# Performance work log

Measured on AMD Instinct MI355X. Metric: run time of the kernel, lower is better.

The kernel has to match this reference:

```python
import jax, jax.numpy as jnp
import numpy as np

B, C, H, W = 8, 112, 64, 64
O, K, G = 112, 3, 14
STRIDE, PAD = 1, 1
K2 = K * K


def setup_inputs() -> dict:
    key = jax.random.key(0)
    ks = jax.random.split(key, 5)
    return {
        "x": jax.random.normal(ks[0], (B, C, H, W), jnp.float32),
        # offset/mask generator conv (3x3, stride 1, pad 1) -> 3*G*K2 channels
        "pg_weight": jax.random.normal(ks[1], (3 * G * K2, C, 3, 3), jnp.float32) * 0.01,
        "pg_bias": jax.random.normal(ks[2], (3 * G * K2,), jnp.float32) * 0.01,
        # main deformable-conv weight [O, C/groups, K, K] (groups=1) and bias
        "weight": jax.random.normal(ks[3], (O, C, K, K), jnp.float32) * 0.05,
        "bias": jax.random.normal(ks[4], (O,), jnp.float32) * 0.01,
    }


def _bilinear_sample(img, y, x):
    # img: [Cg, H, W]; y, x: [K2, Ho, Wo] float sampling coords.
    # Out-of-bounds corners contribute zero (torchvision semantics).
    Hi, Wi = img.shape[1], img.shape[2]
    y0 = jnp.floor(y)
    x0 = jnp.floor(x)

    def corner(yy, xx):
        valid = (yy >= 0) & (yy <= Hi - 1) & (xx >= 0) & (xx <= Wi - 1)
        yc = jnp.clip(yy, 0, Hi - 1).astype(jnp.int32)
        xc = jnp.clip(xx, 0, Wi - 1).astype(jnp.int32)
        v = img[:, yc, xc]  # [Cg, K2, Ho, Wo]
        return jnp.where(valid[None], v, jnp.zeros((), img.dtype))

    wy1 = (y - y0)[None]
    wx1 = (x - x0)[None]
    wy0 = 1.0 - wy1
    wx0 = 1.0 - wx1
    return (corner(y0, x0) * wy0 * wx0
            + corner(y0, x0 + 1) * wy0 * wx1
            + corner(y0 + 1, x0) * wy1 * wx0
            + corner(y0 + 1, x0 + 1) * wy1 * wx1)


def reference(x, pg_weight, pg_bias, weight, bias):
    Bn, Cn, Hn, Wn = x.shape
    Ho = (Hn + 2 * PAD - K) // STRIDE + 1
    Wo = (Wn + 2 * PAD - K) // STRIDE + 1
    # param_generator: 3x3 conv, stride 1, pad 1
    pg = jax.lax.conv_general_dilated(
        x, pg_weight, (1, 1), ((1, 1), (1, 1)),
        dimension_numbers=("NCHW", "OIHW", "NCHW"))
    pg = pg + pg_bias[None, :, None, None]
    GK2 = G * K2
    oh, ow, m = pg[:, :GK2], pg[:, GK2:2 * GK2], pg[:, 2 * GK2:]
    # module concatenates [oh, ow]; deform_conv2d interprets channels as [G, K2, (dy, dx)]
    off = jnp.concatenate([oh, ow], axis=1).reshape(Bn, G, K2, 2, Ho, Wo)
    dy, dx = off[:, :, :, 0], off[:, :, :, 1]
    mask = jax.nn.sigmoid(m).reshape(Bn, G, K2, Ho, Wo)
    # base sampling grid per kernel tap (row-major K*K order)
    ky = (jnp.arange(K2) // K).astype(x.dtype)
    kx = (jnp.arange(K2) % K).astype(x.dtype)
    py = (jnp.arange(Ho, dtype=x.dtype) * STRIDE - PAD)[None, :, None] + ky[:, None, None]
    px = (jnp.arange(Wo, dtype=x.dtype) * STRIDE - PAD)[None, None, :] + kx[:, None, None]
    ys = py[None, None] + dy  # [B, G, K2, Ho, Wo]
    xs = px[None, None] + dx
    xg = x.reshape(Bn, G, Cn // G, Hn, Wn)
    # vmap over batch, then offset group
    sampled = jax.vmap(jax.vmap(_bilinear_sample))(xg, ys, xs)  # [B, G, Cg, K2, Ho, Wo]
    sampled = sampled * mask[:, :, None]
    sampled = sampled.reshape(Bn, Cn, K2, Ho, Wo)
    out = jnp.einsum("bckhw,ock->bohw", sampled, weight.reshape(weight.shape[0], Cn, K2))
    return out + bias[None, :, None, None]
```

## Files before the change

### kernel.cpp

```cpp
#include <hip/hip_runtime.h>
#include <math.h>

#define Bn 8
#define Cn 112
#define Hn 64
#define Wn 64
#define On 112
#define Gn 14
#define PGC 378
#define HW 4096
#define CKW 1008
#define KP 1024
#define NP 384
#define XROW 4356
#define PG_MT 137
#define MPAD (PG_MT * 256)
#define PLANE_ROWS 34848
#define XGUARD 67
#define XTG_ROWS_TOTAL 558080

typedef __attribute__((ext_vector_type(8))) short bf16x8;
typedef __attribute__((ext_vector_type(4))) float f32x4;

__device__ __forceinline__ unsigned short f2bf(float f) {
    union { float f; unsigned int u; } v; v.f = f;
    unsigned int r = v.u + 0x7fffu + ((v.u >> 16) & 1u);
    return (unsigned short)(r >> 16);
}
__device__ __forceinline__ float bf2f(unsigned short u) {
    union { unsigned int u; float f; } v; v.u = ((unsigned int)u) << 16;
    return v.f;
}
__device__ __forceinline__ float bflo(unsigned int u) {
    union { unsigned int u; float f; } v; v.u = u << 16; return v.f;
}
__device__ __forceinline__ float bfhi(unsigned int u) {
    union { unsigned int u; float f; } v; v.u = u & 0xffff0000u; return v.f;
}
__device__ __forceinline__ void gload_lds16(const void* g, void* l) {
    __builtin_amdgcn_global_load_lds(
        (const __attribute__((address_space(1))) unsigned int*)g,
        (__attribute__((address_space(3))) unsigned int*)l, 16, 0, 0);
}

#define ZN XTG_ROWS_TOTAL
#define B2N (NP * KP)
#define WBN (128 * KP)
__global__ __launch_bounds__(256) void prep_kernel(
    const float* __restrict__ pgw, const float* __restrict__ w,
    unsigned short* __restrict__ XTGa, unsigned short* __restrict__ B2,
    unsigned short* __restrict__ WB)
{
    int t = blockIdx.x * 256 + threadIdx.x;
    if (t < ZN) {
        const uint4 z = {0, 0, 0, 0};
        reinterpret_cast<uint4*>(XTGa)[t] = z;
        return;
    }
    t -= ZN;
    if (t < B2N) {
        int oc = t >> 10, ck = t & 1023;
        int pg_ = ck >> 3, cc = ck & 7;
        int tap = pg_ / 14, pl = pg_ % 14;
        float v = (pg_ < 126 && oc < PGC)
            ? pgw[(size_t)oc * CKW + (pl * 8 + cc) * 9 + tap] : 0.f;
        B2[t] = f2bf(v);
        return;
    }
    t -= B2N;
    if (t < WBN) {
        int oc = t >> 10, ck = t & 1023;
        float v = 0.f;
        if (oc < On && ck < CKW) {
            int g = ck / 72, r = ck % 72;
            int k = r >> 3, cc = r & 7;
            v = w[(size_t)oc * CKW + (g * 8 + cc) * 9 + k];
        }
        WB[t] = f2bf(v);
    }
}

__global__ __launch_bounds__(256) void xpose_kernel(
    const float* __restrict__ x, unsigned short* __restrict__ XTG)
{
    __shared__ unsigned short lds[64][136];

    const int tid = threadIdx.x;
    const int y = blockIdx.x, b = blockIdx.y;
    const int xx = tid & 63, cw = tid >> 6;

    const float* xb = x + (size_t)b * Cn * HW + y * 64;
    #pragma unroll
    for (int p = 0; p < 28; ++p) {
        int c = p * 4 + cw;
        lds[xx][c] = f2bf(xb[(size_t)c * HW + xx]);
    }
    __syncthreads();

    #pragma unroll
    for (int q = 0; q < 4; ++q) {
        int task = q * 256 + tid;
        if (task < 896) {
            int g = task >> 6;
            int x2 = task & 63;
            unsigned short* dst = XTG + ((size_t)g * PLANE_ROWS
                + (size_t)b * XROW + (y + 1) * 66 + x2 + 1) * 8;
            *reinterpret_cast<uint4*>(dst) =
                *reinterpret_cast<const uint4*>(&lds[x2][g * 8]);
        }
    }
}

#define A_BUF_B 16384
#define B_BUF_B 8192
__global__ __launch_bounds__(512, 4) void pg_shift_kernel(
    const unsigned short* __restrict__ XTG, const unsigned short* __restrict__ B2,
    const float* __restrict__ pgb, unsigned short* __restrict__ pgBF)
{
    __shared__ __align__(16) unsigned char smem[3 * (A_BUF_B + B_BUF_B)];

    const int tid  = threadIdx.x;
    const int lane = tid & 63;
    const int w    = tid >> 6;
    const int wr   = w >> 1;
    const int wc   = w & 1;
    const int m0   = blockIdx.x * 256;
    const int n0   = blockIdx.y * 128;
    const int fr   = lane & 15, fq = lane >> 4;

    f32x4 acc[4][4] = {};

    auto Abuf = [&](int b) -> unsigned char* { return smem + b * A_BUF_B; };
    auto Bbuf = [&](int b) -> unsigned char* {
        return smem + 3 * A_BUF_B + b * B_BUF_B; };

    auto stage = [&](int buf, int kt) {
        #pragma unroll
        for (int s = 0; s < 2; ++s) {
            int r = w * 32 + s * 16 + (lane >> 2);
            int ch = (lane & 3) ^ ((r >> 1) & 3);
            int pg_ = kt * 4 + ch;
            int tap = pg_ / 14, pl = pg_ % 14;
            int shift = (tap / 3 - 1) * 66 + (tap % 3) - 1;
            if (pg_ >= 126) { pl = 14; shift = 0; }
            gload_lds16(XTG + ((long)pl * PLANE_ROWS + (long)(m0 + r) + shift) * 8,
                        Abuf(buf) + (w * 32 + s * 16) * 64);
        }
        {
            int r = w * 16 + (lane >> 2);
            int ch = (lane & 3) ^ ((r >> 1) & 3);
            gload_lds16(&B2[(size_t)(n0 + r) * KP + kt * 32 + ch * 8],
                        Bbuf(buf) + (w * 16) * 64);
        }
    };

    stage(0, 0);
    stage(1, 1);

    for (int kt = 0; kt < 32; ++kt) {
        if (kt < 31) asm volatile("s_waitcnt vmcnt(3)" ::: "memory");
        else         asm volatile("s_waitcnt vmcnt(0)" ::: "memory");
        __builtin_amdgcn_s_barrier();
        asm volatile("" ::: "memory");

        const int cur = kt % 3;
        const unsigned char* Ab = Abuf(cur);
        const unsigned char* Bb = Bbuf(cur);

        bf16x8 a[4], b[4];
        #pragma unroll
        for (int mi = 0; mi < 4; ++mi) {
            int r = wr * 64 + mi * 16 + fr;
            a[mi] = *reinterpret_cast<const bf16x8*>(
                Ab + r * 64 + ((fq ^ ((r >> 1) & 3)) << 4));
        }
        #pragma unroll
        for (int ni = 0; ni < 4; ++ni) {
            int r = wc * 64 + ni * 16 + fr;
            b[ni] = *reinterpret_cast<const bf16x8*>(
                Bb + r * 64 + ((fq ^ ((r >> 1) & 3)) << 4));
        }
        if (kt + 2 < 32) stage((kt + 2) % 3, kt + 2);

        __builtin_amdgcn_s_setprio(1);
        #pragma unroll
        for (int mi = 0; mi < 4; ++mi)
            #pragma unroll
            for (int ni = 0; ni < 4; ++ni)
                acc[mi][ni] = __builtin_amdgcn_mfma_f32_16x16x32_bf16(
                    a[mi], b[ni], acc[mi][ni], 0, 0, 0);
        __builtin_amdgcn_s_setprio(0);
    }

    __builtin_amdgcn_s_barrier();
    unsigned short* T = (unsigned short*)smem;

    #pragma unroll
    for (int ni = 0; ni < 4; ++ni) {
        int ocl = wc * 64 + ni * 16 + fr;
        float bv = (n0 + ocl < PGC) ? pgb[n0 + ocl] : 0.f;
        #pragma unroll
        for (int mi = 0; mi < 4; ++mi) {
            int pxl = wr * 64 + mi * 16 + fq * 4;
            ushort4 pk;
            pk.x = f2bf(acc[mi][ni][0] + bv);
            pk.y = f2bf(acc[mi][ni][1] + bv);
            pk.z = f2bf(acc[mi][ni][2] + bv);
            pk.w = f2bf(acc[mi][ni][3] + bv);
            *reinterpret_cast<ushort4*>(&T[ocl * 264 + pxl]) = pk;
        }
    }
    __builtin_amdgcn_s_barrier();

    const int pxls = tid & 255;
    const int half = tid >> 8;
    const int pxd  = m0 + pxls;
    const int bb   = pxd / XROW;
    const int rem  = pxd - bb * XROW;
    const int yy   = rem / 66 - 1;
    const int xx   = rem - (yy + 1) * 66 - 1;
    const bool valid = (pxd < Bn * XROW) &&
                       ((unsigned)yy < 64u) && ((unsigned)xx < 64u);
    unsigned short* pbase = pgBF + (size_t)bb * PGC * HW + yy * 64 + xx;

    #pragma unroll 4
    for (int oc = 0; oc < 64; ++oc) {
        int ocg = n0 + half * 64 + oc;
        if (ocg >= PGC) break;
        unsigned short v = T[(half * 64 + oc) * 264 + pxls];
        if (valid) pbase[(size_t)ocg * HW] = v;
    }
}

__global__ __launch_bounds__(256, 4) void fused_kernel(
    const unsigned short* __restrict__ XTG, const unsigned short* __restrict__ pg,
    const unsigned short* __restrict__ WB, const float* __restrict__ bias,
    float* __restrict__ out)
{
    __shared__ __align__(16) unsigned char Ab[2][32 * 128];
    __shared__ __align__(16) unsigned char Bb[2][128 * 128];

    const int tid  = threadIdx.x;
    const int lane = tid & 63;
    const int w    = tid >> 6;
    const int fr   = lane & 15, fq = lane >> 4;

    const int bid = (int)blockIdx.x;
    const int blk = (bid & 7) * 128 + (bid >> 3);
    const int px0 = blk * 32;
    const int b   = px0 >> 12;
    const int hw0 = px0 & 4095;

    const int spx = tid & 31;
    const int q   = tid >> 5;
    const int hw  = hw0 + spx;
    const int sy  = hw >> 6, sx = hw & 63;

    const unsigned short* pgb = pg + (size_t)b * PGC * HW + hw;

    f32x4 acc[2][2] = {};

    unsigned short rdy, rdx, rmv;
    float fdy, fdx, fmv;
    uint4 q00, q01, q10, q11;
    float w00, w01, w10, w11;

    auto issue_pg = [&](int kt) {
        int gk = kt * 8 + q;
        int gkc = min(gk, 125);
        int g = gkc / 9, k = gkc - 9 * g;
        rdy = pgb[(size_t)(18 * g + 2 * k) * HW];
        rdx = pgb[(size_t)(18 * g + 2 * k + 1) * HW];
        rmv = pgb[(size_t)(252 + 9 * g + k) * HW];
    };

    auto issue_gather = [&](int kt1) {
        int gk = kt1 * 8 + q;
        bool valid = gk < 126;
        int gkc = min(gk, 125);
        int g = gkc / 9, k = gkc - 9 * g;
        const int ky = k / 3, kx = k - 3 * ky;
        float m = valid ? 1.f / (1.f + __expf(-fmv)) : 0.f;
        float yf = (float)(sy + ky - 1) + fdy;
        float xf = (float)(sx + kx - 1) + fdx;
        float y0 = floorf(yf), x0 = floorf(xf);
        float wy1 = yf - y0, wx1 = xf - x0;
        float wy0 = 1.f - wy1, wx0 = 1.f - wx1;
        int iy0 = (int)y0, ix0 = (int)x0;
        bool vy0 = (iy0 >= 0) && (iy0 < Hn);
        bool vy1 = (iy0 >= -1) && (iy0 < Hn - 1);
        bool vx0 = (ix0 >= 0) && (ix0 < Wn);
        bool vx1 = (ix0 >= -1) && (ix0 < Wn - 1);
        int cy0 = min(max(iy0, 0), Hn - 1), cy1 = min(max(iy0 + 1, 0), Hn - 1);
        int cx0 = min(max(ix0, 0), Wn - 1), cx1 = min(max(ix0 + 1, 0), Wn - 1);
        w00 = (vy0 && vx0) ? wy0 * wx0 * m : 0.f;
        w01 = (vy0 && vx1) ? wy0 * wx1 * m : 0.f;
        w10 = (vy1 && vx0) ? wy1 * wx0 * m : 0.f;
        w11 = (vy1 && vx1) ? wy1 * wx1 * m : 0.f;
        const unsigned short* xg = XTG +
            ((size_t)g * PLANE_ROWS + (size_t)b * XROW) * 8;
        q00 = *reinterpret_cast<const uint4*>(xg + (size_t)((cy0 + 1) * 66 + cx0 + 1) * 8);
        q01 = *reinterpret_cast<const uint4*>(xg + (size_t)((cy0 + 1) * 66 + cx1 + 1) * 8);
        q10 = *reinterpret_cast<const uint4*>(xg + (size_t)((cy1 + 1) * 66 + cx0 + 1) * 8);
        q11 = *reinterpret_cast<const uint4*>(xg + (size_t)((cy1 + 1) * 66 + cx1 + 1) * 8);
    };

    auto combine_write = [&](int buf) {
        unsigned int c00[4] = {q00.x, q00.y, q00.z, q00.w};
        unsigned int c01[4] = {q01.x, q01.y, q01.z, q01.w};
        unsigned int c10[4] = {q10.x, q10.y, q10.z, q10.w};
        unsigned int c11[4] = {q11.x, q11.y, q11.z, q11.w};
        unsigned int pk[4];
        #pragma unroll
        for (int j = 0; j < 4; ++j) {
            float lo = bflo(c00[j]) * w00 + bflo(c01[j]) * w01 +
                       bflo(c10[j]) * w10 + bflo(c11[j]) * w11;
            float hi = bfhi(c00[j]) * w00 + bfhi(c01[j]) * w01 +
                       bfhi(c10[j]) * w10 + bfhi(c11[j]) * w11;
            pk[j] = (unsigned int)f2bf(lo) | ((unsigned int)f2bf(hi) << 16);
        }
        int slot = q ^ (spx & 7);
        *reinterpret_cast<uint4*>(Ab[buf] + spx * 128 + slot * 16) =
            *reinterpret_cast<const uint4*>(pk);
    };

    auto stageB = [&](int buf, int kt) {
        #pragma unroll
        for (int s = 0; s < 4; ++s) {
            int r = s * 32 + w * 8 + (lane >> 3);
            int ch = (lane & 7) ^ (r & 7);
            gload_lds16(&WB[(size_t)r * KP + kt * 64 + ch * 8],
                        Bb[buf] + (s * 32 + w * 8) * 128);
        }
    };

    auto mfma_tile = [&](int c) {
        #pragma unroll
        for (int ks = 0; ks < 2; ++ks) {
            bf16x8 a[2], bfr[2];
            #pragma unroll
            for (int mi = 0; mi < 2; ++mi) {
                int r = mi * 16 + fr;
                a[mi] = *reinterpret_cast<const bf16x8*>(
                    Ab[c] + r * 128 + (((ks * 4 + fq) ^ (r & 7)) << 4));
            }
            #pragma unroll
            for (int ni = 0; ni < 2; ++ni) {
                int r = w * 32 + ni * 16 + fr;
                bfr[ni] = *reinterpret_cast<const bf16x8*>(
                    Bb[c] + r * 128 + (((ks * 4 + fq) ^ (r & 7)) << 4));
            }
            __builtin_amdgcn_s_setprio(1);
            #pragma unroll
            for (int mi = 0; mi < 2; ++mi)
                #pragma unroll
                for (int ni = 0; ni < 2; ++ni)
                    acc[mi][ni] = __builtin_amdgcn_mfma_f32_16x16x32_bf16(
                        a[mi], bfr[ni], acc[mi][ni], 0, 0, 0);
            __builtin_amdgcn_s_setprio(0);
        }
    };

    issue_pg(0);
    asm volatile("s_waitcnt vmcnt(0)" ::: "memory");
    fdy = bf2f(rdy); fdx = bf2f(rdx); fmv = bf2f(rmv);
    issue_gather(0);
    asm volatile("" ::: "memory");
    stageB(0, 0);
    asm volatile("" ::: "memory");
    issue_pg(1);
    asm volatile("s_waitcnt vmcnt(7)" ::: "memory");
    combine_write(0);
    asm volatile("s_waitcnt vmcnt(0)" ::: "memory");
    fdy = bf2f(rdy); fdx = bf2f(rdx); fmv = bf2f(rmv);
    asm volatile("s_waitcnt lgkmcnt(0)" ::: "memory");
    __builtin_amdgcn_s_barrier();
    asm volatile("" ::: "memory");

    int cur = 0;
    for (int kt = 0; kt < 16; ++kt) {
        if (kt < 15) {
            issue_gather(kt + 1);
            asm volatile("" ::: "memory");
            stageB(cur ^ 1, kt + 1);
            asm volatile("" ::: "memory");
            issue_pg(min(kt + 2, 15));
            asm volatile("" ::: "memory");
        }
        mfma_tile(cur);
        if (kt < 15) {
            asm volatile("s_waitcnt vmcnt(7)" ::: "memory");
            combine_write(cur ^ 1);
            asm volatile("s_waitcnt vmcnt(0)" ::: "memory");
            fdy = bf2f(rdy); fdx = bf2f(rdx); fmv = bf2f(rmv);
            asm volatile("s_waitcnt lgkmcnt(0)" ::: "memory");
            __builtin_amdgcn_s_barrier();
            asm volatile("" ::: "memory");
            cur ^= 1;
        }
    }

    #pragma unroll
    for (int ni = 0; ni < 2; ++ni) {
        int oc = w * 32 + ni * 16 + fr;
        if (oc >= On) continue;
        float bv = bias[oc];
        #pragma unroll
        for (int mi = 0; mi < 2; ++mi) {
            int hwo = hw0 + mi * 16 + fq * 4;
            float4 o;
            o.x = acc[mi][ni][0] + bv;
            o.y = acc[mi][ni][1] + bv;
            o.z = acc[mi][ni][2] + bv;
            o.w = acc[mi][ni][3] + bv;
            *reinterpret_cast<float4*>(
                &out[((size_t)(b * On + oc)) * HW + hwo]) = o;
        }
    }
}

extern "C" void kernel_launch(void* const* d_in, const int* in_sizes, int n_in,
                              void* d_out, int out_size, void* d_ws, size_t ws_size,
                              hipStream_t stream) {
    const float* x    = (const float*)d_in[0];
    const float* pgw  = (const float*)d_in[1];
    const float* pgb  = (const float*)d_in[2];
    const float* w    = (const float*)d_in[3];
    const float* bias = (const float*)d_in[4];
    float* out = (float*)d_out;

    char* wsb = (char*)d_ws;
    unsigned short* pgBF = (unsigned short*)wsb;
    size_t off = (size_t)PGC * Bn * HW * 2;
    unsigned short* B2   = (unsigned short*)(wsb + off);
    off += (size_t)NP * KP * 2;
    unsigned short* WB   = (unsigned short*)(wsb + off);
    off += (size_t)128 * KP * 2;
    unsigned short* XTGa = (unsigned short*)(wsb + off);
    unsigned short* XTG  = XTGa + (size_t)XGUARD * 8;

    {
        int tot = ZN + B2N + WBN;
        prep_kernel<<<(tot + 255) / 256, 256, 0, stream>>>(pgw, w, XTGa, B2, WB);
    }
    xpose_kernel<<<dim3(Hn, Bn), 256, 0, stream>>>(x, XTG);

    pg_shift_kernel<<<dim3(PG_MT, NP / 128), 512, 0, stream>>>(
        XTG, B2, pgb, pgBF);

    fused_kernel<<<dim3(1024), 256, 0, stream>>>(XTG, pgBF, WB, bias, out);
}
```

Measured before the change: 91.97 us.

## Double-buffer pg GEMM pipeline and split epilogue to cut LDS for occupancy

Changes the pg_shift_kernel from a 3-stage to a 2-stage LDS ring, shrinking shared memory from 72KB to 48KB, and raises the launch-bounds occupancy hint from 4 to 6. The epilogue now stages output through LDS in two halves, one per column-wave group, so the transpose buffer fits in the smaller allocation. The aim is more resident blocks per CU to hide latency. The cost is less prefetch depth, an extra barrier per K iteration, more barriers in the epilogue, and possible register pressure from the tighter bound.

```diff
diff --git a/kernel.cpp b/kernel.cpp
--- a/kernel.cpp
+++ b/kernel.cpp
@@ -113,11 +113,11 @@
 
 #define A_BUF_B 16384
 #define B_BUF_B 8192
-__global__ __launch_bounds__(512, 4) void pg_shift_kernel(
+__global__ __launch_bounds__(512, 6) void pg_shift_kernel(
     const unsigned short* __restrict__ XTG, const unsigned short* __restrict__ B2,
     const float* __restrict__ pgb, unsigned short* __restrict__ pgBF)
 {
-    __shared__ __align__(16) unsigned char smem[3 * (A_BUF_B + B_BUF_B)];
+    __shared__ __align__(16) unsigned char smem[2 * (A_BUF_B + B_BUF_B)];
 
     const int tid  = threadIdx.x;
     const int lane = tid & 63;
@@ -132,7 +132,7 @@
 
     auto Abuf = [&](int b) -> unsigned char* { return smem + b * A_BUF_B; };
     auto Bbuf = [&](int b) -> unsigned char* {
-        return smem + 3 * A_BUF_B + b * B_BUF_B; };
+        return smem + 2 * A_BUF_B + b * B_BUF_B; };
 
     auto stage = [&](int buf, int kt) {
         #pragma unroll
@@ -155,15 +155,17 @@
     };
 
     stage(0, 0);
-    stage(1, 1);
-
+    int cur = 0;
     for (int kt = 0; kt < 32; ++kt) {
-        if (kt < 31) asm volatile("s_waitcnt vmcnt(3)" ::: "memory");
-        else         asm volatile("s_waitcnt vmcnt(0)" ::: "memory");
+        if (kt + 1 < 32) {
+            stage(cur ^ 1, kt + 1);
+            asm volatile("s_waitcnt vmcnt(3)" ::: "memory");
+        } else {
+            asm volatile("s_waitcnt vmcnt(0)" ::: "memory");
+        }
         __builtin_amdgcn_s_barrier();
         asm volatile("" ::: "memory");
 
-        const int cur = kt % 3;
         const unsigned char* Ab = Abuf(cur);
         const unsigned char* Bb = Bbuf(cur);
 
@@ -180,7 +182,6 @@
             b[ni] = *reinterpret_cast<const bf16x8*>(
                 Bb + r * 64 + ((fq ^ ((r >> 1) & 3)) << 4));
         }
-        if (kt + 2 < 32) stage((kt + 2) % 3, kt + 2);
 
         __builtin_amdgcn_s_setprio(1);
         #pragma unroll
@@ -190,30 +191,17 @@
                 acc[mi][ni] = __builtin_amdgcn_mfma_f32_16x16x32_bf16(
                     a[mi], b[ni], acc[mi][ni], 0, 0, 0);
         __builtin_amdgcn_s_setprio(0);
-    }
-
-    __builtin_amdgcn_s_barrier();
+
+        asm volatile("s_waitcnt lgkmcnt(0)" ::: "memory");
+        __builtin_amdgcn_s_barrier();
+        asm volatile("" ::: "memory");
+        cur ^= 1;
+    }
+
     unsigned short* T = (unsigned short*)smem;
 
-    #pragma unroll
-    for (int ni = 0; ni < 4; ++ni) {
-        int ocl = wc * 64 + ni * 16 + fr;
-        float bv = (n0 + ocl < PGC) ? pgb[n0 + ocl] : 0.f;
-        #pragma unroll
-        for (int mi = 0; mi < 4; ++mi) {
-            int pxl = wr * 64 + mi * 16 + fq * 4;
-            ushort4 pk;
-            pk.x = f2bf(acc[mi][ni][0] + bv);
-            pk.y = f2bf(acc[mi][ni][1] + bv);
-            pk.z = f2bf(acc[mi][ni][2] + bv);
-            pk.w = f2bf(acc[mi][ni][3] + bv);
-            *reinterpret_cast<ushort4*>(&T[ocl * 264 + pxl]) = pk;
-        }
-    }
-    __builtin_amdgcn_s_barrier();
-
     const int pxls = tid & 255;
-    const int half = tid >> 8;
+    const int ho   = tid >> 8;
     const int pxd  = m0 + pxls;
     const int bb   = pxd / XROW;
     const int rem  = pxd - bb * XROW;
@@ -223,12 +211,38 @@
                        ((unsigned)yy < 64u) && ((unsigned)xx < 64u);
     unsigned short* pbase = pgBF + (size_t)bb * PGC * HW + yy * 64 + xx;
 
-    #pragma unroll 4
-    for (int oc = 0; oc < 64; ++oc) {
-        int ocg = n0 + half * 64 + oc;
-        if (ocg >= PGC) break;
-        unsigned short v = T[(half * 64 + oc) * 264 + pxls];
-        if (valid) pbase[(size_t)ocg * HW] = v;
+    #pragma unroll
+    for (int h = 0; h < 2; ++h) {
+        if (wc == h) {
+            #pragma unroll
+            for (int ni = 0; ni < 4; ++ni) {
+                int ocl = ni * 16 + fr;
+                int ocg = n0 + h * 64 + ocl;
+                float bv = (ocg < PGC) ? pgb[ocg] : 0.f;
+                #pragma unroll
+                for (int mi = 0; mi < 4; ++mi) {
+                    int pxl = wr * 64 + mi * 16 + fq * 4;
+                    ushort4 pk;
+                    pk.x = f2bf(acc[mi][ni][0] + bv);
+                    pk.y = f2bf(acc[mi][ni][1] + bv);
+                    pk.z = f2bf(acc[mi][ni][2] + bv);
+                    pk.w = f2bf(acc[mi][ni][3] + bv);
+                    *reinterpret_cast<ushort4*>(&T[ocl * 264 + pxl]) = pk;
+                }
+            }
+        }
+        __builtin_amdgcn_s_barrier();
+        #pragma unroll 4
+        for (int j = 0; j < 32; ++j) {
+            int ocg = n0 + h * 64 + ho * 32 + j;
+            if (ocg < PGC) {
+                unsigned short v = T[(ho * 32 + j) * 264 + pxls];
+                if (valid) pbase[(size_t)ocg * HW] = v;
+            }
+        }
+        if (h == 0) {
+            __builtin_amdgcn_s_barrier();
+        }
     }
 }
 
```

Measured after the change: 291.2 us. +216.6%, slower.
